# Kernel optimization log

Hardware: AMD Instinct MI355X
Metric: run time of the kernel (lower is better)

The kernel has to match this reference:

```python
import jax, jax.numpy as jnp
import numpy as np

DIM = 256
FFN_DIM = 512
NH = 8
EPS = 1e-5


def ln(x, g, b):
    m = x.mean(-1, keepdims=True)
    v = ((x - m) ** 2).mean(-1, keepdims=True)
    return (x - m) / jnp.sqrt(v + EPS) * g + b


def setup_inputs() -> dict:
    key = jax.random.key(0)
    ks = jax.random.split(key, 16)
    B, L, C, H, W = 16, 16384, DIM, 128, 128
    s = 0.02
    return {
        "query": jax.random.normal(ks[0], (B, 1, C), jnp.float32),
        "mem": jax.random.normal(ks[1], (B, L, C), jnp.float32),
        "ior_emb": jax.random.uniform(ks[2], (B, NH, H, W), jnp.float32),
        # input_proj: Linear(dim,dim) + ReLU + LayerNorm
        "W_ip": jax.random.normal(ks[3], (C, C), jnp.float32) * s,
        "b_ip": jnp.zeros((C,), jnp.float32),
        "g_ip": jnp.ones((C,), jnp.float32),
        "be_ip": jnp.zeros((C,), jnp.float32),
        # q / kv projections
        "W_q": jax.random.normal(ks[4], (C, C), jnp.float32) * s,
        "b_q": jnp.zeros((C,), jnp.float32),
        "W_kv": jax.random.normal(ks[5], (C, 2 * C), jnp.float32) * s,
        "b_kv": jnp.zeros((2 * C,), jnp.float32),
        # norm_q, norm_ffn
        "g_q": jnp.ones((C,), jnp.float32),
        "be_q": jnp.zeros((C,), jnp.float32),
        "g_f": jnp.ones((C,), jnp.float32),
        "be_f": jnp.zeros((C,), jnp.float32),
        # ffn (Mlp)
        "W1": jax.random.normal(ks[6], (C, FFN_DIM), jnp.float32) * s,
        "b1": jnp.zeros((FFN_DIM,), jnp.float32),
        "W2": jax.random.normal(ks[7], (FFN_DIM, C), jnp.float32) * s,
        "b2": jnp.zeros((C,), jnp.float32),
    }


def reference(query, mem, ior_emb, W_ip, b_ip, g_ip, be_ip, W_q, b_q, W_kv, b_kv,
              g_q, be_q, g_f, be_f, W1, b1, W2, b2):
    B, L, C = mem.shape
    nh = ior_emb.shape[1]
    hd = C // nh
    scale = hd ** -0.5
    # input_proj(mem): Linear -> ReLU -> LayerNorm
    m = ln(jax.nn.relu(mem @ W_ip + b_ip), g_ip, be_ip)  # [B,L,C]
    kv = m @ W_kv + b_kv
    k, v = kv[..., :C], kv[..., C:]
    q = ln(query, g_q, be_q) @ W_q + b_q  # [B,1,C]
    # per-head split along channel == reshape (..., nh, hd)
    qh = q.reshape(B, 1, nh, hd)
    kh = k.reshape(B, L, nh, hd)
    vh = v.reshape(B, L, nh, hd)
    ior = ior_emb.reshape(B, nh, 1, L)
    scores = jnp.einsum('bqhd,blhd->bhql', qh, kh) * scale * ior  # [B,nh,1,L]
    attn = jax.nn.softmax(scores, axis=-1)
    out = jnp.einsum('bhql,blhd->bqhd', attn, vh).reshape(B, 1, C)
    x = out + query
    h = ln(x, g_f, be_f)
    ffn = jax.nn.gelu(h @ W1 + b1, approximate=False) @ W2 + b2
    return x + ffn
```

## Files before the change

kernel.cpp:

```cpp
#include <hip/hip_runtime.h>
#include <math.h>

#define CDIM 256
#define LDIM 16384
#define NH 8
#define HD 32
#define FFN 512
#define EPS 1e-5f
#define SCALE 0.17677669529663687f

#define RB 64
#define NCHUNK 256
#define LDA 264
#define PSTRIDE 258

typedef __attribute__((ext_vector_type(8))) short short8;
typedef __attribute__((ext_vector_type(4))) float f32x4;

union U8 { short8 s8; unsigned u[4]; };

__device__ inline unsigned short f2bf(float x) {
    unsigned int u = __float_as_uint(x);
    unsigned int lsb = (u >> 16) & 1u;
    u += 0x7fffu + lsb;
    return (unsigned short)(u >> 16);
}


__global__ __launch_bounds__(256) void convert_weights(const float* __restrict__ Wip,
                                                       unsigned short* __restrict__ w1) {
    int idx = blockIdx.x * 256 + threadIdx.x;
    int j = idx & 7, l = (idx >> 3) & 63, c = (idx >> 9) & 15, t = idx >> 13;
    int k = t * 32 + (l >> 4) * 8 + j;
    int colc = c * 16 + (l & 15);
    w1[idx] = f2bf(Wip[k * CDIM + colc]);
}


__global__ __launch_bounds__(256) void qprep_kernel(const float* __restrict__ query,
                                                    const float* __restrict__ Wq,
                                                    const float* __restrict__ bq,
                                                    const float* __restrict__ gq,
                                                    const float* __restrict__ beq,
                                                    const float* __restrict__ Wkv,
                                                    const float* __restrict__ bkv,
                                                    float* __restrict__ qs,
                                                    unsigned short* __restrict__ wts,
                                                    float* __restrict__ qcb) {
    int b = blockIdx.x;
    int tid = threadIdx.x;
    int wave = tid >> 6, lane = tid & 63;
    __shared__ float sh[CDIM];
    __shared__ float qsh[CDIM];
    __shared__ float red[8];

    float x = query[b * CDIM + tid];
    float s = x, sq = x * x;
#pragma unroll
    for (int m = 32; m >= 1; m >>= 1) { s += __shfl_xor(s, m, 64); sq += __shfl_xor(sq, m, 64); }
    if (lane == 0) { red[wave] = s; red[4 + wave] = sq; }
    __syncthreads();
    float ts = red[0] + red[1] + red[2] + red[3];
    float tq = red[4] + red[5] + red[6] + red[7];
    float mean = ts * (1.f / CDIM);
    float var = tq * (1.f / CDIM) - mean * mean;
    float rstd = rsqrtf(var + EPS);
    sh[tid] = (x - mean) * rstd * gq[tid] + beq[tid];
    __syncthreads();

    float acc = bq[tid];
    for (int k = 0; k < CDIM; ++k) acc = fmaf(sh[k], Wq[k * CDIM + tid], acc);
    float qv = acc * SCALE;
    qs[b * CDIM + tid] = qv;
    qsh[tid] = qv;
    __syncthreads();

    float wa[8];
#pragma unroll
    for (int h = 0; h < 8; ++h) wa[h] = 0.f;
    const float* wr = Wkv + (size_t)tid * (2 * CDIM);
#pragma unroll
    for (int h = 0; h < 8; ++h)
#pragma unroll
        for (int d = 0; d < 32; ++d)
            wa[h] = fmaf(wr[h * 32 + d], qsh[h * 32 + d], wa[h]);
    unsigned short* wb = wts + (b << 12) + ((tid >> 5) << 9) + (((tid >> 3) & 3) << 7) + (tid & 7);
#pragma unroll
    for (int h = 0; h < 8; ++h) wb[h << 3] = f2bf(wa[h]);
#pragma unroll
    for (int h = 8; h < 16; ++h) wb[h << 3] = 0;

    if (tid < 16) {
        float cb = 0.f;
        if (tid < 8) {
#pragma unroll
            for (int d = 0; d < 32; ++d) cb = fmaf(bkv[tid * 32 + d], qsh[tid * 32 + d], cb);
        }
        qcb[b * 16 + tid] = cb;
    }
}


__device__ inline void mfma_gemm(const unsigned short* __restrict__ smA,
                                 const unsigned short* __restrict__ wsw, int NC, int ctile0,
                                 int lx, int quad, f32x4 acc[4][4]) {
#pragma unroll
    for (int rt = 0; rt < 4; ++rt)
#pragma unroll
        for (int ci = 0; ci < 4; ++ci) acc[rt][ci] = (f32x4){0.f, 0.f, 0.f, 0.f};

    int l = quad * 16 + lx;
#pragma unroll
    for (int t = 0; t < 8; ++t) {
        short8 bfrag[4];
#pragma unroll
        for (int ci = 0; ci < 4; ++ci)
            bfrag[ci] = *(const short8*)(wsw + (((size_t)(t * NC + ctile0 + ci)) * 64 + l) * 8);
        short8 afrag[4];
#pragma unroll
        for (int rt = 0; rt < 4; ++rt)
            afrag[rt] = *(const short8*)(smA + (rt * 16 + lx) * LDA + t * 32 + quad * 8);
#pragma unroll
        for (int rt = 0; rt < 4; ++rt)
#pragma unroll
            for (int ci = 0; ci < 4; ++ci)
                acc[rt][ci] = __builtin_amdgcn_mfma_f32_16x16x32_bf16(afrag[rt], bfrag[ci], acc[rt][ci], 0, 0, 0);
    }
}


__device__ inline void mfma_svec(const unsigned short* __restrict__ smA,
                                 const unsigned short* __restrict__ wt,
                                 int lx, int quad, f32x4 accS[4]) {
#pragma unroll
    for (int rt = 0; rt < 4; ++rt) accS[rt] = (f32x4){0.f, 0.f, 0.f, 0.f};
    int l = quad * 16 + lx;
#pragma unroll
    for (int t = 0; t < 8; ++t) {
        short8 bf = *(const short8*)(wt + ((t * 64 + l) << 3));
        short8 af[4];
#pragma unroll
        for (int rt = 0; rt < 4; ++rt)
            af[rt] = *(const short8*)(smA + (rt * 16 + lx) * LDA + t * 32 + quad * 8);
#pragma unroll
        for (int rt = 0; rt < 4; ++rt)
            accS[rt] = __builtin_amdgcn_mfma_f32_16x16x32_bf16(af[rt], bf, accS[rt], 0, 0, 0);
    }
}


__global__ __launch_bounds__(256, 4) void main_kernel(const float* __restrict__ mem,
                                                      const unsigned short* __restrict__ w1,
                                                      const unsigned short* __restrict__ wts,
                                                      const float* __restrict__ bip,
                                                      const float* __restrict__ gip,
                                                      const float* __restrict__ beip,
                                                      const float* __restrict__ qcb,
                                                      const float* __restrict__ ior,
                                                      float* __restrict__ partials) {
    int blk = blockIdx.x;
    int b = blk >> 8;
    int chunk = blk & 255;
    int row0 = chunk * RB;
    int tid = threadIdx.x;
    int w = tid >> 6, lane = tid & 63;
    int quad = lane >> 4, lx = lane & 15;

    __shared__ unsigned short bufA[RB * LDA];
    __shared__ float iorS[NH][66];
    __shared__ float redS[4][RB];
    __shared__ float redQ[4][RB];
    __shared__ float stats[2][RB];

    {
        int i0 = tid, i1 = tid + 256;
        iorS[i0 >> 6][i0 & 63] = ior[((size_t)(b * NH + (i0 >> 6))) * LDIM + row0 + (i0 & 63)];
        iorS[i1 >> 6][i1 & 63] = ior[((size_t)(b * NH + (i1 >> 6))) * LDIM + row0 + (i1 & 63)];
    }
    {
        const float4* src = (const float4*)(mem + ((size_t)b * LDIM + row0) * CDIM);
#pragma unroll
        for (int it = 0; it < 16; ++it) {
            int i = tid + 256 * it;
            int r = i >> 6, c4 = i & 63;
            float4 v = src[i];
            ushort4 u;
            u.x = f2bf(v.x); u.y = f2bf(v.y); u.z = f2bf(v.z); u.w = f2bf(v.w);
            *(ushort4*)&bufA[r * LDA + c4 * 4] = u;
        }
    }
    __syncthreads();

    int col[4];
#pragma unroll
    for (int ci = 0; ci < 4; ++ci) col[ci] = (4 * w + ci) * 16 + lx;

    f32x4 acc[4][4];
    mfma_gemm(bufA, w1, 16, 4 * w, lx, quad, acc);

    float bb[4], gg[4], ee[4];
#pragma unroll
    for (int ci = 0; ci < 4; ++ci) { bb[ci] = bip[col[ci]]; gg[ci] = gip[col[ci]]; ee[ci] = beip[col[ci]]; }

#pragma unroll
    for (int rt = 0; rt < 4; ++rt) {
#pragma unroll
        for (int reg = 0; reg < 4; ++reg) {
#pragma unroll
            for (int ci = 0; ci < 4; ++ci)
                acc[rt][ci][reg] = fmaxf(acc[rt][ci][reg] + bb[ci], 0.f);
            float s2 = acc[rt][0][reg] + acc[rt][1][reg] + acc[rt][2][reg] + acc[rt][3][reg];
            float q2 = acc[rt][0][reg] * acc[rt][0][reg] + acc[rt][1][reg] * acc[rt][1][reg]
                     + acc[rt][2][reg] * acc[rt][2][reg] + acc[rt][3][reg] * acc[rt][3][reg];
#pragma unroll
            for (int m = 8; m >= 1; m >>= 1) { s2 += __shfl_xor(s2, m, 64); q2 += __shfl_xor(q2, m, 64); }
            if (lx == 0) {
                int row = rt * 16 + quad * 4 + reg;
                redS[w][row] = s2;
                redQ[w][row] = q2;
            }
        }
    }
    __syncthreads();
    if (tid < RB) {
        float s2 = redS[0][tid] + redS[1][tid] + redS[2][tid] + redS[3][tid];
        float q2 = redQ[0][tid] + redQ[1][tid] + redQ[2][tid] + redQ[3][tid];
        float mean = s2 * (1.f / CDIM);
        float var = q2 * (1.f / CDIM) - mean * mean;
        stats[0][tid] = mean;
        stats[1][tid] = rsqrtf(var + EPS);
    }
    __syncthreads();

    unsigned ypk0[4][4], ypk1[4][4];
#pragma unroll
    for (int rt = 0; rt < 4; ++rt) {
        float mn[4], rs[4];
#pragma unroll
        for (int reg = 0; reg < 4; ++reg) {
            int row = rt * 16 + quad * 4 + reg;
            mn[reg] = stats[0][row];
            rs[reg] = stats[1][row];
        }
#pragma unroll
        for (int ci = 0; ci < 4; ++ci) {
            unsigned short u0 = f2bf((acc[rt][ci][0] - mn[0]) * rs[0] * gg[ci] + ee[ci]);
            unsigned short u1 = f2bf((acc[rt][ci][1] - mn[1]) * rs[1] * gg[ci] + ee[ci]);
            unsigned short u2 = f2bf((acc[rt][ci][2] - mn[2]) * rs[2] * gg[ci] + ee[ci]);
            unsigned short u3 = f2bf((acc[rt][ci][3] - mn[3]) * rs[3] * gg[ci] + ee[ci]);
            int rbase = rt * 16 + quad * 4;
            bufA[(rbase + 0) * LDA + col[ci]] = u0;
            bufA[(rbase + 1) * LDA + col[ci]] = u1;
            bufA[(rbase + 2) * LDA + col[ci]] = u2;
            bufA[(rbase + 3) * LDA + col[ci]] = u3;
            ypk0[rt][ci] = (unsigned)u0 | ((unsigned)u1 << 16);
            ypk1[rt][ci] = (unsigned)u2 | ((unsigned)u3 << 16);
        }
    }
    __syncthreads();

    f32x4 accS[4];
    mfma_svec(bufA, wts + ((size_t)b << 12), lx, quad, accS);

    float qcv = qcb[(b << 4) + lx];
    float p[16];
    float cmax = -1e30f;
#pragma unroll
    for (int rt = 0; rt < 4; ++rt)
#pragma unroll
        for (int reg = 0; reg < 4; ++reg) {
            int row = rt * 16 + quad * 4 + reg;
            float sc = (accS[rt][reg] + qcv) * iorS[lx & 7][row];
            p[rt * 4 + reg] = sc;
            cmax = fmaxf(cmax, sc);
        }
    cmax = fmaxf(cmax, __shfl_xor(cmax, 16, 64));
    cmax = fmaxf(cmax, __shfl_xor(cmax, 32, 64));
    float csum = 0.f;
#pragma unroll
    for (int i = 0; i < 16; ++i) { p[i] = __expf(p[i] - cmax); csum += p[i]; }
    csum += __shfl_xor(csum, 16, 64);
    csum += __shfl_xor(csum, 32, 64);

    f32x4 accPV[4];
#pragma unroll
    for (int ci = 0; ci < 4; ++ci) accPV[ci] = (f32x4){0.f, 0.f, 0.f, 0.f};

    int srcA = ((quad & 1) << 5) + lx;
    int srcB = srcA + 16;
    bool hiQ = quad >= 2;
#pragma unroll
    for (int t2 = 0; t2 < 2; ++t2) {
        float pe[8];
#pragma unroll
        for (int jj = 0; jj < 4; ++jj) {
            float v0 = __shfl(p[t2 * 8 + jj], srcA, 64);
            float v1 = __shfl(p[t2 * 8 + 4 + jj], srcA, 64);
            pe[jj] = hiQ ? v1 : v0;
            float v2 = __shfl(p[t2 * 8 + jj], srcB, 64);
            float v3 = __shfl(p[t2 * 8 + 4 + jj], srcB, 64);
            pe[4 + jj] = hiQ ? v3 : v2;
        }
        U8 pa;
        pa.u[0] = (unsigned)f2bf(pe[0]) | ((unsigned)f2bf(pe[1]) << 16);
        pa.u[1] = (unsigned)f2bf(pe[2]) | ((unsigned)f2bf(pe[3]) << 16);
        pa.u[2] = (unsigned)f2bf(pe[4]) | ((unsigned)f2bf(pe[5]) << 16);
        pa.u[3] = (unsigned)f2bf(pe[6]) | ((unsigned)f2bf(pe[7]) << 16);

#pragma unroll
        for (int ci = 0; ci < 4; ++ci) {
            unsigned a0 = (unsigned)__shfl((int)ypk0[t2 * 2][ci], srcA, 64);
            unsigned b0 = (unsigned)__shfl((int)ypk0[t2 * 2 + 1][ci], srcA, 64);
            unsigned a1 = (unsigned)__shfl((int)ypk1[t2 * 2][ci], srcA, 64);
            unsigned b1 = (unsigned)__shfl((int)ypk1[t2 * 2 + 1][ci], srcA, 64);
            unsigned a2 = (unsigned)__shfl((int)ypk0[t2 * 2][ci], srcB, 64);
            unsigned b2 = (unsigned)__shfl((int)ypk0[t2 * 2 + 1][ci], srcB, 64);
            unsigned a3 = (unsigned)__shfl((int)ypk1[t2 * 2][ci], srcB, 64);
            unsigned b3 = (unsigned)__shfl((int)ypk1[t2 * 2 + 1][ci], srcB, 64);
            U8 ub;
            ub.u[0] = hiQ ? b0 : a0;
            ub.u[1] = hiQ ? b1 : a1;
            ub.u[2] = hiQ ? b2 : a2;
            ub.u[3] = hiQ ? b3 : a3;
            accPV[ci] = __builtin_amdgcn_mfma_f32_16x16x32_bf16(pa.s8, ub.s8, accPV[ci], 0, 0, 0);
        }
    }

    size_t pb = ((size_t)(b * NCHUNK + chunk)) * NH * PSTRIDE;
    if (quad < 2) {
#pragma unroll
        for (int reg = 0; reg < 4; ++reg) {
            float* dst = partials + pb + (size_t)(quad * 4 + reg) * PSTRIDE;
#pragma unroll
            for (int ci = 0; ci < 4; ++ci) dst[col[ci]] = accPV[ci][reg];
        }
    }
    if (quad == 0 && lx < 8) {
        float* dst = partials + pb + (size_t)lx * PSTRIDE;
        dst[256] = cmax;
        dst[257] = csum;
    }
}


__global__ __launch_bounds__(256) void combine_kernel(const float* __restrict__ partials,
                                                      const float* __restrict__ Wkv,
                                                      const float* __restrict__ bkv,
                                                      float* __restrict__ attnout) {
    int bh = blockIdx.x;
    int b = bh >> 3, h = bh & 7;
    int tid = threadIdx.x;
    __shared__ float ms[NCHUNK], wf[NCHUNK], mt[CDIM];
    __shared__ float sredA[4];
    __shared__ float ored[8][33];

    const float* base = partials + ((size_t)b * NCHUNK * NH + h) * PSTRIDE;
    ms[tid] = base[(size_t)tid * NH * PSTRIDE + 256];
    __syncthreads();
    float M = -1e30f;
    for (int s = 0; s < NCHUNK; ++s) M = fmaxf(M, ms[s]);
    float e = __expf(ms[tid] - M);
    wf[tid] = e;
    float Sl = base[(size_t)tid * NH * PSTRIDE + 257] * e;
#pragma unroll
    for (int m = 32; m >= 1; m >>= 1) Sl += __shfl_xor(Sl, m, 64);
    if ((tid & 63) == 0) sredA[tid >> 6] = Sl;
    __syncthreads();
    float St = sredA[0] + sredA[1] + sredA[2] + sredA[3];

    float acc = 0.f;
    for (int s = 0; s < NCHUNK; ++s) acc = fmaf(wf[s], base[(size_t)s * NH * PSTRIDE + tid], acc);
    mt[tid] = acc / St;
    __syncthreads();

    int d = tid & 31, g = tid >> 5;
    float a2 = 0.f;
    for (int c = g * 32; c < g * 32 + 32; ++c)
        a2 = fmaf(mt[c], Wkv[(size_t)c * (2 * CDIM) + CDIM + h * 32 + d], a2);
    ored[g][d] = a2;
    __syncthreads();
    if (tid < 32) {
        float o = bkv[CDIM + h * 32 + tid];
#pragma unroll
        for (int gg2 = 0; gg2 < 8; ++gg2) o += ored[gg2][tid];
        attnout[b * CDIM + h * HD + tid] = o;
    }
}


__global__ __launch_bounds__(256) void epilogue_kernel(const float* __restrict__ attnout,
                                                       const float* __restrict__ query,
                                                       const float* __restrict__ gf,
                                                       const float* __restrict__ bef,
                                                       const float* __restrict__ W1,
                                                       const float* __restrict__ b1,
                                                       const float* __restrict__ W2,
                                                       const float* __restrict__ b2,
                                                       float* __restrict__ out) {
    int b = blockIdx.x;
    int tid = threadIdx.x;
    int wave = tid >> 6, lane = tid & 63;
    __shared__ float sh[FFN];
    __shared__ float red[8];

    float x = attnout[b * CDIM + tid] + query[b * CDIM + tid];
    float s = x, sq = x * x;
#pragma unroll
    for (int m = 32; m >= 1; m >>= 1) { s += __shfl_xor(s, m, 64); sq += __shfl_xor(sq, m, 64); }
    if (lane == 0) { red[wave] = s; red[4 + wave] = sq; }
    __syncthreads();
    float ts = red[0] + red[1] + red[2] + red[3];
    float tq = red[4] + red[5] + red[6] + red[7];
    float mean = ts * (1.f / CDIM);
    float var = tq * (1.f / CDIM) - mean * mean;
    float rstd = rsqrtf(var + EPS);
    sh[tid] = (x - mean) * rstd * gf[tid] + bef[tid];
    __syncthreads();

    float t[2];
#pragma unroll
    for (int i = 0; i < 2; ++i) {
        int f = tid + 256 * i;
        float a = b1[f];
        for (int k = 0; k < CDIM; ++k) a = fmaf(sh[k], W1[k * FFN + f], a);
        t[i] = 0.5f * a * (1.f + erff(a * 0.7071067811865476f));
    }
    __syncthreads();
    sh[tid] = t[0];
    sh[tid + 256] = t[1];
    __syncthreads();

    float y = b2[tid];
    for (int f = 0; f < FFN; ++f) y = fmaf(sh[f], W2[f * CDIM + tid], y);
    out[b * CDIM + tid] = x + y;
}


extern "C" void kernel_launch(void* const* d_in, const int* in_sizes, int n_in,
                              void* d_out, int out_size, void* d_ws, size_t ws_size,
                              hipStream_t stream) {
    const float* query = (const float*)d_in[0];
    const float* mem   = (const float*)d_in[1];
    const float* ior   = (const float*)d_in[2];
    const float* Wip   = (const float*)d_in[3];
    const float* bip   = (const float*)d_in[4];
    const float* gip   = (const float*)d_in[5];
    const float* beip  = (const float*)d_in[6];
    const float* Wq    = (const float*)d_in[7];
    const float* bq    = (const float*)d_in[8];
    const float* Wkv   = (const float*)d_in[9];
    const float* bkv   = (const float*)d_in[10];
    const float* gq    = (const float*)d_in[11];
    const float* beq   = (const float*)d_in[12];
    const float* gf    = (const float*)d_in[13];
    const float* bef   = (const float*)d_in[14];
    const float* W1    = (const float*)d_in[15];
    const float* b1    = (const float*)d_in[16];
    const float* W2    = (const float*)d_in[17];
    const float* b2    = (const float*)d_in[18];
    float* out = (float*)d_out;

    char* ws = (char*)d_ws;
    float* qs             = (float*)(ws);
    float* attnout        = (float*)(ws + 16384);
    float* qcb            = (float*)(ws + 32768);
    unsigned short* w1sw  = (unsigned short*)(ws + 33792);
    unsigned short* wtsw  = (unsigned short*)(ws + 164864);
    float* partials       = (float*)(ws + 295936);

    const int B = 16;

    convert_weights<<<256, 256, 0, stream>>>(Wip, w1sw);
    qprep_kernel<<<B, 256, 0, stream>>>(query, Wq, bq, gq, beq, Wkv, bkv, qs, wtsw, qcb);
    main_kernel<<<B * NCHUNK, 256, 0, stream>>>(mem, w1sw, wtsw, bip, gip, beip, qcb, ior, partials);
    combine_kernel<<<B * NH, 256, 0, stream>>>(partials, Wkv, bkv, attnout);
    epilogue_kernel<<<B, 256, 0, stream>>>(attnout, query, gf, bef, W1, b1, W2, b2, out);
}
```

Before: 526.5 us.

## Make main kernel persistent over chunks with double-buffered prefetch and swizzled LDS

Each block now processes 8 consecutive 64-row chunks instead of one, prefetching the next chunk's mem and ior into registers while computing the current one and writing them into a second LDS buffer. LDS row padding is replaced by an XOR swizzle so the double buffer fits without bank conflicts. The partials layout is split into a head-major PV array and a separate max/sum array so the combine kernel reads contiguously. This trades a grid 8x smaller (512 blocks) and no minimum-occupancy hint for latency hiding of the mem stream, risking lower occupancy from the 64 extra prefetch registers.

```diff
diff --git a/kernel.cpp b/kernel.cpp
--- a/kernel.cpp
+++ b/kernel.cpp
@@ -11,8 +11,8 @@
 
 #define RB 64
 #define NCHUNK 256
-#define LDA 264
-#define PSTRIDE 258
+#define CPB 8
+#define NGRP 32
 
 typedef __attribute__((ext_vector_type(8))) short short8;
 typedef __attribute__((ext_vector_type(4))) float f32x4;
@@ -110,16 +110,19 @@
         for (int ci = 0; ci < 4; ++ci) acc[rt][ci] = (f32x4){0.f, 0.f, 0.f, 0.f};
 
     int l = quad * 16 + lx;
+    int xv = (lx & 7) << 4;
+    const char* base = (const char*)smA;
 #pragma unroll
     for (int t = 0; t < 8; ++t) {
         short8 bfrag[4];
 #pragma unroll
         for (int ci = 0; ci < 4; ++ci)
             bfrag[ci] = *(const short8*)(wsw + (((size_t)(t * NC + ctile0 + ci)) * 64 + l) * 8);
+        int cb = (t * 64 + quad * 16) ^ xv;
         short8 afrag[4];
 #pragma unroll
         for (int rt = 0; rt < 4; ++rt)
-            afrag[rt] = *(const short8*)(smA + (rt * 16 + lx) * LDA + t * 32 + quad * 8);
+            afrag[rt] = *(const short8*)(base + (rt * 16 + lx) * 512 + cb);
 #pragma unroll
         for (int rt = 0; rt < 4; ++rt)
 #pragma unroll
@@ -127,7 +130,6 @@
                 acc[rt][ci] = __builtin_amdgcn_mfma_f32_16x16x32_bf16(afrag[rt], bfrag[ci], acc[rt][ci], 0, 0, 0);
     }
 }
-
 
 __device__ inline void mfma_svec(const unsigned short* __restrict__ smA,
                                  const unsigned short* __restrict__ wt,
@@ -135,215 +137,251 @@
 #pragma unroll
     for (int rt = 0; rt < 4; ++rt) accS[rt] = (f32x4){0.f, 0.f, 0.f, 0.f};
     int l = quad * 16 + lx;
+    int xv = (lx & 7) << 4;
+    const char* base = (const char*)smA;
 #pragma unroll
     for (int t = 0; t < 8; ++t) {
         short8 bf = *(const short8*)(wt + ((t * 64 + l) << 3));
+        int cb = (t * 64 + quad * 16) ^ xv;
         short8 af[4];
 #pragma unroll
         for (int rt = 0; rt < 4; ++rt)
-            af[rt] = *(const short8*)(smA + (rt * 16 + lx) * LDA + t * 32 + quad * 8);
+            af[rt] = *(const short8*)(base + (rt * 16 + lx) * 512 + cb);
 #pragma unroll
         for (int rt = 0; rt < 4; ++rt)
             accS[rt] = __builtin_amdgcn_mfma_f32_16x16x32_bf16(af[rt], bf, accS[rt], 0, 0, 0);
     }
 }
 
-
-__global__ __launch_bounds__(256, 4) void main_kernel(const float* __restrict__ mem,
-                                                      const unsigned short* __restrict__ w1,
-                                                      const unsigned short* __restrict__ wts,
-                                                      const float* __restrict__ bip,
-                                                      const float* __restrict__ gip,
-                                                      const float* __restrict__ beip,
-                                                      const float* __restrict__ qcb,
-                                                      const float* __restrict__ ior,
-                                                      float* __restrict__ partials) {
+__device__ inline void cw(unsigned short* bufc, int tid, int it, float4 v) {
+    int i = tid + (it << 8);
+    int r = i >> 6, c4 = i & 63;
+    int cb = (c4 << 3) ^ ((r & 7) << 4);
+    ushort4 u;
+    u.x = f2bf(v.x); u.y = f2bf(v.y); u.z = f2bf(v.z); u.w = f2bf(v.w);
+    *(ushort4*)((char*)bufc + r * 512 + cb) = u;
+}
+
+
+__global__ __launch_bounds__(256) void main_kernel(const float* __restrict__ mem,
+                                                   const unsigned short* __restrict__ w1,
+                                                   const unsigned short* __restrict__ wts,
+                                                   const float* __restrict__ bip,
+                                                   const float* __restrict__ gip,
+                                                   const float* __restrict__ beip,
+                                                   const float* __restrict__ qcb,
+                                                   const float* __restrict__ ior,
+                                                   float* __restrict__ mpart,
+                                                   float* __restrict__ msum) {
     int blk = blockIdx.x;
-    int b = blk >> 8;
-    int chunk = blk & 255;
-    int row0 = chunk * RB;
+    int b = blk >> 5;
+    int g = blk & 31;
+    int chunk0 = g * CPB;
     int tid = threadIdx.x;
     int w = tid >> 6, lane = tid & 63;
     int quad = lane >> 4, lx = lane & 15;
 
-    __shared__ unsigned short bufA[RB * LDA];
-    __shared__ float iorS[NH][66];
+    __shared__ unsigned short bufA[2][RB * 256];
+    __shared__ float iorS[2][NH][66];
     __shared__ float redS[4][RB];
     __shared__ float redQ[4][RB];
     __shared__ float stats[2][RB];
 
+    int col[4];
+#pragma unroll
+    for (int ci = 0; ci < 4; ++ci) col[ci] = (4 * w + ci) * 16 + lx;
+    float bb[4], gg[4], ee[4];
+#pragma unroll
+    for (int ci = 0; ci < 4; ++ci) { bb[ci] = bip[col[ci]]; gg[ci] = gip[col[ci]]; ee[ci] = beip[col[ci]]; }
+    float qcv = qcb[(b << 4) + lx];
+    const unsigned short* wtb = wts + ((size_t)b << 12);
+
+    int ih = tid >> 6, ir = tid & 63;
+
     {
-        int i0 = tid, i1 = tid + 256;
-        iorS[i0 >> 6][i0 & 63] = ior[((size_t)(b * NH + (i0 >> 6))) * LDIM + row0 + (i0 & 63)];
-        iorS[i1 >> 6][i1 & 63] = ior[((size_t)(b * NH + (i1 >> 6))) * LDIM + row0 + (i1 & 63)];
-    }
-    {
-        const float4* src = (const float4*)(mem + ((size_t)b * LDIM + row0) * CDIM);
-#pragma unroll
-        for (int it = 0; it < 16; ++it) {
-            int i = tid + 256 * it;
-            int r = i >> 6, c4 = i & 63;
-            float4 v = src[i];
-            ushort4 u;
-            u.x = f2bf(v.x); u.y = f2bf(v.y); u.z = f2bf(v.z); u.w = f2bf(v.w);
-            *(ushort4*)&bufA[r * LDA + c4 * 4] = u;
-        }
-    }
-    __syncthreads();
-
-    int col[4];
-#pragma unroll
-    for (int ci = 0; ci < 4; ++ci) col[ci] = (4 * w + ci) * 16 + lx;
-
-    f32x4 acc[4][4];
-    mfma_gemm(bufA, w1, 16, 4 * w, lx, quad, acc);
-
-    float bb[4], gg[4], ee[4];
-#pragma unroll
-    for (int ci = 0; ci < 4; ++ci) { bb[ci] = bip[col[ci]]; gg[ci] = gip[col[ci]]; ee[ci] = beip[col[ci]]; }
-
-#pragma unroll
-    for (int rt = 0; rt < 4; ++rt) {
-#pragma unroll
-        for (int reg = 0; reg < 4; ++reg) {
-#pragma unroll
-            for (int ci = 0; ci < 4; ++ci)
-                acc[rt][ci][reg] = fmaxf(acc[rt][ci][reg] + bb[ci], 0.f);
-            float s2 = acc[rt][0][reg] + acc[rt][1][reg] + acc[rt][2][reg] + acc[rt][3][reg];
-            float q2 = acc[rt][0][reg] * acc[rt][0][reg] + acc[rt][1][reg] * acc[rt][1][reg]
-                     + acc[rt][2][reg] * acc[rt][2][reg] + acc[rt][3][reg] * acc[rt][3][reg];
-#pragma unroll
-            for (int m = 8; m >= 1; m >>= 1) { s2 += __shfl_xor(s2, m, 64); q2 += __shfl_xor(q2, m, 64); }
-            if (lx == 0) {
+        const float4* src = (const float4*)(mem + ((size_t)b * LDIM + (size_t)chunk0 * RB) * CDIM);
+        float4 v[16];
+#pragma unroll
+        for (int it = 0; it < 16; ++it) v[it] = src[tid + (it << 8)];
+        float pi0 = ior[((size_t)(b * NH + ih)) * LDIM + chunk0 * RB + ir];
+        float pi1 = ior[((size_t)(b * NH + 4 + ih)) * LDIM + chunk0 * RB + ir];
+#pragma unroll
+        for (int it = 0; it < 16; ++it) cw(&bufA[0][0], tid, it, v[it]);
+        iorS[0][ih][ir] = pi0;
+        iorS[0][4 + ih][ir] = pi1;
+    }
+
+#pragma unroll 1
+    for (int i = 0; i < CPB; ++i) {
+        int cur = i & 1, nxt = cur ^ 1;
+        int chunk = chunk0 + i;
+        bool pf = (i + 1 < CPB);
+        __syncthreads();
+
+        float4 va[16];
+        float rn0 = 0.f, rn1 = 0.f;
+        if (pf) {
+            const float4* srcn = (const float4*)(mem + ((size_t)b * LDIM + (size_t)(chunk + 1) * RB) * CDIM);
+#pragma unroll
+            for (int it = 0; it < 16; ++it) va[it] = srcn[tid + (it << 8)];
+            rn0 = ior[((size_t)(b * NH + ih)) * LDIM + (size_t)(chunk + 1) * RB + ir];
+            rn1 = ior[((size_t)(b * NH + 4 + ih)) * LDIM + (size_t)(chunk + 1) * RB + ir];
+        }
+
+        f32x4 acc[4][4];
+        mfma_gemm(&bufA[cur][0], w1, 16, 4 * w, lx, quad, acc);
+
+#pragma unroll
+        for (int rt = 0; rt < 4; ++rt) {
+#pragma unroll
+            for (int reg = 0; reg < 4; ++reg) {
+#pragma unroll
+                for (int ci = 0; ci < 4; ++ci)
+                    acc[rt][ci][reg] = fmaxf(acc[rt][ci][reg] + bb[ci], 0.f);
+                float s2 = acc[rt][0][reg] + acc[rt][1][reg] + acc[rt][2][reg] + acc[rt][3][reg];
+                float q2 = acc[rt][0][reg] * acc[rt][0][reg] + acc[rt][1][reg] * acc[rt][1][reg]
+                         + acc[rt][2][reg] * acc[rt][2][reg] + acc[rt][3][reg] * acc[rt][3][reg];
+#pragma unroll
+                for (int m = 8; m >= 1; m >>= 1) { s2 += __shfl_xor(s2, m, 64); q2 += __shfl_xor(q2, m, 64); }
+                if (lx == 0) {
+                    int row = rt * 16 + quad * 4 + reg;
+                    redS[w][row] = s2;
+                    redQ[w][row] = q2;
+                }
+            }
+        }
+        __syncthreads();
+        if (tid < RB) {
+            float s2 = redS[0][tid] + redS[1][tid] + redS[2][tid] + redS[3][tid];
+            float q2 = redQ[0][tid] + redQ[1][tid] + redQ[2][tid] + redQ[3][tid];
+            float mean = s2 * (1.f / CDIM);
+            float var = q2 * (1.f / CDIM) - mean * mean;
+            stats[0][tid] = mean;
+            stats[1][tid] = rsqrtf(var + EPS);
+        }
+        if (pf) {
+#pragma unroll
+            for (int it = 0; it < 16; ++it) cw(&bufA[nxt][0], tid, it, va[it]);
+            iorS[nxt][ih][ir] = rn0;
+            iorS[nxt][4 + ih][ir] = rn1;
+        }
+        __syncthreads();
+
+        unsigned ypk0[4][4], ypk1[4][4];
+        char* bufc = (char*)&bufA[cur][0];
+#pragma unroll
+        for (int rt = 0; rt < 4; ++rt) {
+            float mn[4], rs[4];
+#pragma unroll
+            for (int reg = 0; reg < 4; ++reg) {
                 int row = rt * 16 + quad * 4 + reg;
-                redS[w][row] = s2;
-                redQ[w][row] = q2;
-            }
-        }
-    }
-    __syncthreads();
-    if (tid < RB) {
-        float s2 = redS[0][tid] + redS[1][tid] + redS[2][tid] + redS[3][tid];
-        float q2 = redQ[0][tid] + redQ[1][tid] + redQ[2][tid] + redQ[3][tid];
-        float mean = s2 * (1.f / CDIM);
-        float var = q2 * (1.f / CDIM) - mean * mean;
-        stats[0][tid] = mean;
-        stats[1][tid] = rsqrtf(var + EPS);
-    }
-    __syncthreads();
-
-    unsigned ypk0[4][4], ypk1[4][4];
-#pragma unroll
-    for (int rt = 0; rt < 4; ++rt) {
-        float mn[4], rs[4];
-#pragma unroll
-        for (int reg = 0; reg < 4; ++reg) {
-            int row = rt * 16 + quad * 4 + reg;
-            mn[reg] = stats[0][row];
-            rs[reg] = stats[1][row];
-        }
-#pragma unroll
-        for (int ci = 0; ci < 4; ++ci) {
-            unsigned short u0 = f2bf((acc[rt][ci][0] - mn[0]) * rs[0] * gg[ci] + ee[ci]);
-            unsigned short u1 = f2bf((acc[rt][ci][1] - mn[1]) * rs[1] * gg[ci] + ee[ci]);
-            unsigned short u2 = f2bf((acc[rt][ci][2] - mn[2]) * rs[2] * gg[ci] + ee[ci]);
-            unsigned short u3 = f2bf((acc[rt][ci][3] - mn[3]) * rs[3] * gg[ci] + ee[ci]);
-            int rbase = rt * 16 + quad * 4;
-            bufA[(rbase + 0) * LDA + col[ci]] = u0;
-            bufA[(rbase + 1) * LDA + col[ci]] = u1;
-            bufA[(rbase + 2) * LDA + col[ci]] = u2;
-            bufA[(rbase + 3) * LDA + col[ci]] = u3;
-            ypk0[rt][ci] = (unsigned)u0 | ((unsigned)u1 << 16);
-            ypk1[rt][ci] = (unsigned)u2 | ((unsigned)u3 << 16);
-        }
-    }
-    __syncthreads();
-
-    f32x4 accS[4];
-    mfma_svec(bufA, wts + ((size_t)b << 12), lx, quad, accS);
-
-    float qcv = qcb[(b << 4) + lx];
-    float p[16];
-    float cmax = -1e30f;
-#pragma unroll
-    for (int rt = 0; rt < 4; ++rt)
-#pragma unroll
-        for (int reg = 0; reg < 4; ++reg) {
-            int row = rt * 16 + quad * 4 + reg;
-            float sc = (accS[rt][reg] + qcv) * iorS[lx & 7][row];
-            p[rt * 4 + reg] = sc;
-            cmax = fmaxf(cmax, sc);
-        }
-    cmax = fmaxf(cmax, __shfl_xor(cmax, 16, 64));
-    cmax = fmaxf(cmax, __shfl_xor(cmax, 32, 64));
-    float csum = 0.f;
-#pragma unroll
-    for (int i = 0; i < 16; ++i) { p[i] = __expf(p[i] - cmax); csum += p[i]; }
-    csum += __shfl_xor(csum, 16, 64);
-    csum += __shfl_xor(csum, 32, 64);
-
-    f32x4 accPV[4];
-#pragma unroll
-    for (int ci = 0; ci < 4; ++ci) accPV[ci] = (f32x4){0.f, 0.f, 0.f, 0.f};
-
-    int srcA = ((quad & 1) << 5) + lx;
-    int srcB = srcA + 16;
-    bool hiQ = quad >= 2;
-#pragma unroll
-    for (int t2 = 0; t2 < 2; ++t2) {
-        float pe[8];
-#pragma unroll
-        for (int jj = 0; jj < 4; ++jj) {
-            float v0 = __shfl(p[t2 * 8 + jj], srcA, 64);
-            float v1 = __shfl(p[t2 * 8 + 4 + jj], srcA, 64);
-            pe[jj] = hiQ ? v1 : v0;
-            float v2 = __shfl(p[t2 * 8 + jj], srcB, 64);
-            float v3 = __shfl(p[t2 * 8 + 4 + jj], srcB, 64);
-            pe[4 + jj] = hiQ ? v3 : v2;
-        }
-        U8 pa;
-        pa.u[0] = (unsigned)f2bf(pe[0]) | ((unsigned)f2bf(pe[1]) << 16);
-        pa.u[1] = (unsigned)f2bf(pe[2]) | ((unsigned)f2bf(pe[3]) << 16);
-        pa.u[2] = (unsigned)f2bf(pe[4]) | ((unsigned)f2bf(pe[5]) << 16);
-        pa.u[3] = (unsigned)f2bf(pe[6]) | ((unsigned)f2bf(pe[7]) << 16);
-
-#pragma unroll
-        for (int ci = 0; ci < 4; ++ci) {
-            unsigned a0 = (unsigned)__shfl((int)ypk0[t2 * 2][ci], srcA, 64);
-            unsigned b0 = (unsigned)__shfl((int)ypk0[t2 * 2 + 1][ci], srcA, 64);
-            unsigned a1 = (unsigned)__shfl((int)ypk1[t2 * 2][ci], srcA, 64);
-            unsigned b1 = (unsigned)__shfl((int)ypk1[t2 * 2 + 1][ci], srcA, 64);
-            unsigned a2 = (unsigned)__shfl((int)ypk0[t2 * 2][ci], srcB, 64);
-            unsigned b2 = (unsigned)__shfl((int)ypk0[t2 * 2 + 1][ci], srcB, 64);
-            unsigned a3 = (unsigned)__shfl((int)ypk1[t2 * 2][ci], srcB, 64);
-            unsigned b3 = (unsigned)__shfl((int)ypk1[t2 * 2 + 1][ci], srcB, 64);
-            U8 ub;
-            ub.u[0] = hiQ ? b0 : a0;
-            ub.u[1] = hiQ ? b1 : a1;
-            ub.u[2] = hiQ ? b2 : a2;
-            ub.u[3] = hiQ ? b3 : a3;
-            accPV[ci] = __builtin_amdgcn_mfma_f32_16x16x32_bf16(pa.s8, ub.s8, accPV[ci], 0, 0, 0);
-        }
-    }
-
-    size_t pb = ((size_t)(b * NCHUNK + chunk)) * NH * PSTRIDE;
-    if (quad < 2) {
-#pragma unroll
-        for (int reg = 0; reg < 4; ++reg) {
-            float* dst = partials + pb + (size_t)(quad * 4 + reg) * PSTRIDE;
-#pragma unroll
-            for (int ci = 0; ci < 4; ++ci) dst[col[ci]] = accPV[ci][reg];
-        }
-    }
-    if (quad == 0 && lx < 8) {
-        float* dst = partials + pb + (size_t)lx * PSTRIDE;
-        dst[256] = cmax;
-        dst[257] = csum;
-    }
-}
-
-
-__global__ __launch_bounds__(256) void combine_kernel(const float* __restrict__ partials,
+                mn[reg] = stats[0][row];
+                rs[reg] = stats[1][row];
+            }
+#pragma unroll
+            for (int ci = 0; ci < 4; ++ci) {
+                unsigned short u0 = f2bf((acc[rt][ci][0] - mn[0]) * rs[0] * gg[ci] + ee[ci]);
+                unsigned short u1 = f2bf((acc[rt][ci][1] - mn[1]) * rs[1] * gg[ci] + ee[ci]);
+                unsigned short u2 = f2bf((acc[rt][ci][2] - mn[2]) * rs[2] * gg[ci] + ee[ci]);
+                unsigned short u3 = f2bf((acc[rt][ci][3] - mn[3]) * rs[3] * gg[ci] + ee[ci]);
+                int cb = col[ci] * 2;
+                int rbase = rt * 16 + quad * 4;
+                *(unsigned short*)(bufc + (rbase + 0) * 512 + (cb ^ (((quad * 4 + 0) & 7) << 4))) = u0;
+                *(unsigned short*)(bufc + (rbase + 1) * 512 + (cb ^ (((quad * 4 + 1) & 7) << 4))) = u1;
+                *(unsigned short*)(bufc + (rbase + 2) * 512 + (cb ^ (((quad * 4 + 2) & 7) << 4))) = u2;
+                *(unsigned short*)(bufc + (rbase + 3) * 512 + (cb ^ (((quad * 4 + 3) & 7) << 4))) = u3;
+                ypk0[rt][ci] = (unsigned)u0 | ((unsigned)u1 << 16);
+                ypk1[rt][ci] = (unsigned)u2 | ((unsigned)u3 << 16);
+            }
+        }
+        __syncthreads();
+
+        f32x4 accS[4];
+        mfma_svec(&bufA[cur][0], wtb, lx, quad, accS);
+
+        float pr[16];
+        float cmax = -1e30f;
+#pragma unroll
+        for (int rt = 0; rt < 4; ++rt)
+#pragma unroll
+            for (int reg = 0; reg < 4; ++reg) {
+                int row = rt * 16 + quad * 4 + reg;
+                float sc = (accS[rt][reg] + qcv) * iorS[cur][lx & 7][row];
+                pr[rt * 4 + reg] = sc;
+                cmax = fmaxf(cmax, sc);
+            }
+        cmax = fmaxf(cmax, __shfl_xor(cmax, 16, 64));
+        cmax = fmaxf(cmax, __shfl_xor(cmax, 32, 64));
+        float csum = 0.f;
+#pragma unroll
+        for (int j = 0; j < 16; ++j) { pr[j] = __expf(pr[j] - cmax); csum += pr[j]; }
+        csum += __shfl_xor(csum, 16, 64);
+        csum += __shfl_xor(csum, 32, 64);
+
+        f32x4 accPV[4];
+#pragma unroll
+        for (int ci = 0; ci < 4; ++ci) accPV[ci] = (f32x4){0.f, 0.f, 0.f, 0.f};
+
+        int srcA = ((quad & 1) << 5) + lx;
+        int srcB = srcA + 16;
+        bool hiQ = quad >= 2;
+#pragma unroll
+        for (int t2 = 0; t2 < 2; ++t2) {
+            float pe[8];
+#pragma unroll
+            for (int jj = 0; jj < 4; ++jj) {
+                float v0 = __shfl(pr[t2 * 8 + jj], srcA, 64);
+                float v1 = __shfl(pr[t2 * 8 + 4 + jj], srcA, 64);
+                pe[jj] = hiQ ? v1 : v0;
+                float v2 = __shfl(pr[t2 * 8 + jj], srcB, 64);
+                float v3 = __shfl(pr[t2 * 8 + 4 + jj], srcB, 64);
+                pe[4 + jj] = hiQ ? v3 : v2;
+            }
+            U8 pa;
+            pa.u[0] = (unsigned)f2bf(pe[0]) | ((unsigned)f2bf(pe[1]) << 16);
+            pa.u[1] = (unsigned)f2bf(pe[2]) | ((unsigned)f2bf(pe[3]) << 16);
+            pa.u[2] = (unsigned)f2bf(pe[4]) | ((unsigned)f2bf(pe[5]) << 16);
+            pa.u[3] = (unsigned)f2bf(pe[6]) | ((unsigned)f2bf(pe[7]) << 16);
+
+#pragma unroll
+            for (int ci = 0; ci < 4; ++ci) {
+                unsigned a0 = (unsigned)__shfl((int)ypk0[t2 * 2][ci], srcA, 64);
+                unsigned b0 = (unsigned)__shfl((int)ypk0[t2 * 2 + 1][ci], srcA, 64);
+                unsigned a1 = (unsigned)__shfl((int)ypk1[t2 * 2][ci], srcA, 64);
+                unsigned b1 = (unsigned)__shfl((int)ypk1[t2 * 2 + 1][ci], srcA, 64);
+                unsigned a2 = (unsigned)__shfl((int)ypk0[t2 * 2][ci], srcB, 64);
+                unsigned b2 = (unsigned)__shfl((int)ypk0[t2 * 2 + 1][ci], srcB, 64);
+                unsigned a3 = (unsigned)__shfl((int)ypk1[t2 * 2][ci], srcB, 64);
+                unsigned b3 = (unsigned)__shfl((int)ypk1[t2 * 2 + 1][ci], srcB, 64);
+                U8 ub;
+                ub.u[0] = hiQ ? b0 : a0;
+                ub.u[1] = hiQ ? b1 : a1;
+                ub.u[2] = hiQ ? b2 : a2;
+                ub.u[3] = hiQ ? b3 : a3;
+                accPV[ci] = __builtin_amdgcn_mfma_f32_16x16x32_bf16(pa.s8, ub.s8, accPV[ci], 0, 0, 0);
+            }
+        }
+
+        if (quad < 2) {
+#pragma unroll
+            for (int reg = 0; reg < 4; ++reg) {
+                int h = quad * 4 + reg;
+                float* dst = mpart + ((((size_t)(b * NH + h)) * NCHUNK + chunk) << 8);
+#pragma unroll
+                for (int ci = 0; ci < 4; ++ci) dst[col[ci]] = accPV[ci][reg];
+            }
+        }
+        if (quad == 0 && lx < 8) {
+            float* dst = msum + ((((size_t)(b * NH + lx)) * NCHUNK + chunk) << 1);
+            dst[0] = cmax;
+            dst[1] = csum;
+        }
+    }
+}
+
+
+__global__ __launch_bounds__(256) void combine_kernel(const float* __restrict__ mpart,
+                                                      const float* __restrict__ msum,
                                                       const float* __restrict__ Wkv,
                                                       const float* __restrict__ bkv,
                                                       float* __restrict__ attnout) {
@@ -354,14 +392,15 @@
     __shared__ float sredA[4];
     __shared__ float ored[8][33];
 
-    const float* base = partials + ((size_t)b * NCHUNK * NH + h) * PSTRIDE;
-    ms[tid] = base[(size_t)tid * NH * PSTRIDE + 256];
+    const float* basem = mpart + (((size_t)(b * NH + h)) * NCHUNK << 8);
+    const float* bases = msum + (((size_t)(b * NH + h)) * NCHUNK << 1);
+    ms[tid] = bases[tid << 1];
     __syncthreads();
     float M = -1e30f;
     for (int s = 0; s < NCHUNK; ++s) M = fmaxf(M, ms[s]);
     float e = __expf(ms[tid] - M);
     wf[tid] = e;
-    float Sl = base[(size_t)tid * NH * PSTRIDE + 257] * e;
+    float Sl = bases[(tid << 1) + 1] * e;
 #pragma unroll
     for (int m = 32; m >= 1; m >>= 1) Sl += __shfl_xor(Sl, m, 64);
     if ((tid & 63) == 0) sredA[tid >> 6] = Sl;
@@ -369,7 +408,7 @@
     float St = sredA[0] + sredA[1] + sredA[2] + sredA[3];
 
     float acc = 0.f;
-    for (int s = 0; s < NCHUNK; ++s) acc = fmaf(wf[s], base[(size_t)s * NH * PSTRIDE + tid], acc);
+    for (int s = 0; s < NCHUNK; ++s) acc = fmaf(wf[s], basem[((size_t)s << 8) + tid], acc);
     mt[tid] = acc / St;
     __syncthreads();
 
@@ -466,13 +505,14 @@
     float* qcb            = (float*)(ws + 32768);
     unsigned short* w1sw  = (unsigned short*)(ws + 33792);
     unsigned short* wtsw  = (unsigned short*)(ws + 164864);
-    float* partials       = (float*)(ws + 295936);
+    float* mpart          = (float*)(ws + 295936);
+    float* msum           = (float*)(ws + 295936 + 33554432);
 
     const int B = 16;
 
     convert_weights<<<256, 256, 0, stream>>>(Wip, w1sw);
     qprep_kernel<<<B, 256, 0, stream>>>(query, Wq, bq, gq, beq, Wkv, bkv, qs, wtsw, qcb);
-    main_kernel<<<B * NCHUNK, 256, 0, stream>>>(mem, w1sw, wtsw, bip, gip, beip, qcb, ior, partials);
-    combine_kernel<<<B * NH, 256, 0, stream>>>(partials, Wkv, bkv, attnout);
+    main_kernel<<<B * NGRP, 256, 0, stream>>>(mem, w1sw, wtsw, bip, gip, beip, qcb, ior, mpart, msum);
+    combine_kernel<<<B * NH, 256, 0, stream>>>(mpart, msum, Wkv, bkv, attnout);
     epilogue_kernel<<<B, 256, 0, stream>>>(attnout, query, gf, bef, W1, b1, W2, b2, out);
 }
```

Measured after the change: 593.5 us. 12.7% more time.
